# Kernel tuning notes

Hardware: AMD Instinct MI355X
Metric: run time of the kernel (lower is better)

The kernel has to match this reference:

```python
import jax, jax.numpy as jnp
import numpy as np

N = 100000   # nodes
F = 128      # feature dim (== numEdges ctor arg)
H = 64       # hidden_dim
E = 1600000  # edges (avg degree 16)


def setup_inputs() -> dict:
    key = jax.random.key(0)
    ks = jax.random.split(key, 8)
    x = jax.random.normal(ks[0], (N, F), dtype=jnp.float32)
    edge_index = jax.random.randint(ks[1], (2, E), 0, N)
    sF = 1.0 / np.sqrt(F)
    sH = 1.0 / np.sqrt(H)
    conv_W = jax.random.normal(ks[2], (F, F), dtype=jnp.float32) * sF  # GCNConv linear weight
    conv_b = jnp.zeros((F,), dtype=jnp.float32)
    w1 = jax.random.normal(ks[3], (H, F), dtype=jnp.float32) * sF
    b1 = jnp.zeros((H,), dtype=jnp.float32)
    w2 = jax.random.normal(ks[4], (H, H), dtype=jnp.float32) * sH
    b2 = jnp.zeros((H,), dtype=jnp.float32)
    w3 = jax.random.normal(ks[5], (1, H), dtype=jnp.float32) * sH
    b3 = jnp.zeros((1,), dtype=jnp.float32)
    return dict(x=x, edge_index=edge_index, conv_W=conv_W, conv_b=conv_b,
                w1=w1, b1=b1, w2=w2, b2=b2, w3=w3, b3=b3)


def reference(x, edge_index, conv_W, conv_b, w1, b1, w2, b2, w3, b3):
    n = x.shape[0]
    # --- GCNConv: D^{-1/2}(A+I)D^{-1/2} X W + b ---
    xw = x @ conv_W.T                                   # [N, F]
    loops = jnp.arange(n)
    src = jnp.concatenate([edge_index[0], loops])       # add self-loops
    dst = jnp.concatenate([edge_index[1], loops])
    deg = jax.ops.segment_sum(jnp.ones(src.shape[0], xw.dtype), dst, num_segments=n)
    dinv = jnp.where(deg > 0, jax.lax.rsqrt(deg), 0.0)
    norm = dinv[src] * dinv[dst]                        # [E+N]
    h = jax.ops.segment_sum(xw[src] * norm[:, None], dst, num_segments=n) + conv_b  # [N, F]
    # --- MedianAggregation (index=None -> single segment, 'lower' interpolation) ---
    med = jnp.sort(h, axis=0)[(n - 1) // 2][None, :]    # [1, F]
    # --- tanh MLP ---
    a = jnp.tanh(med @ w1.T + b1)
    a = jnp.tanh(a @ w2.T + b2)
    return a @ w3.T + b3                                # [1, 1]
```

## Files before the change

### kernel.cpp

```cpp
#include <hip/hip_runtime.h>
#include <math.h>


#define CAP    24576
#define CCAP   96
#define DSTR   32
#define OVCAP  4096
#define SPCAP  2048
#define BCAP   4608
#define NBKMAX 400
#define CH     4096

typedef __attribute__((ext_vector_type(8))) short short8;
typedef __attribute__((ext_vector_type(4))) float f32x4;
typedef __attribute__((ext_vector_type(8))) _Float16 half8;
typedef __attribute__((ext_vector_type(2))) _Float16 half2v;

__device__ __forceinline__ unsigned ordKey(float x) {
    unsigned u = __float_as_uint(x);
    return (u & 0x80000000u) ? ~u : (u | 0x80000000u);
}
__device__ __forceinline__ unsigned short f2bf(float f) {
    unsigned u = __float_as_uint(f);
    return (unsigned short)((u + 0x7FFFu + ((u >> 16) & 1u)) >> 16);
}

__global__ void k_init(int* __restrict__ cursor, int* __restrict__ below,
                       int* __restrict__ candCnt, int* __restrict__ ovCnt,
                       const float* __restrict__ W, short* __restrict__ Whi,
                       short* __restrict__ Wlo, int nbk) {
    if (blockIdx.x == 1) {
        for (int idx = threadIdx.x; idx < 16384; idx += 256) {
            int j = idx & 7, lane = (idx >> 3) & 63;
            int t = (idx >> 9) & 7, s = idx >> 12;
            int row = t * 16 + (lane & 15);
            int k = s * 32 + (lane >> 4) * 8 + j;
            float w = W[row * 128 + k];
            unsigned short hb = f2bf(w);
            float hf = __uint_as_float((unsigned)hb << 16);
            Whi[idx] = (short)hb;
            Wlo[idx] = (short)f2bf(w - hf);
        }
        return;
    }
    int t = threadIdx.x;
    for (int i = t; i < nbk; i += 256) cursor[i] = 0;
    if (t < 128) { below[t] = 0; candCnt[t] = 0; }
    if (t == 0) { ovCnt[0] = 0; ovCnt[1] = 0; }
}

__global__ __launch_bounds__(256) void k_binGemm(
        const float* __restrict__ x, const short* __restrict__ Whi,
        const short* __restrict__ Wlo, _Float16* __restrict__ xw, int n, int GB,
        const int* __restrict__ src, const int* __restrict__ dst, int E,
        int* __restrict__ cursor, int2* __restrict__ binned,
        int* __restrict__ ovCnt, int2* __restrict__ ovBuf, int nbk) {
    __shared__ char smem[39168];
    const int t = threadIdx.x;
    if ((int)blockIdx.x < GB) {
        float* trn = (float*)smem;
        const int lane = t & 63, wv = t >> 6;
        const int quad = lane >> 4, m = lane & 15;
        const int rowBase = blockIdx.x * 64 + wv * 16;
        const int r = rowBase + m;
        const int rl = r < n ? r : (n - 1);
        f32x4 acc[8];
        #pragma unroll
        for (int q = 0; q < 8; q++) acc[q] = (f32x4){0.f, 0.f, 0.f, 0.f};
        #pragma unroll
        for (int s = 0; s < 4; s++) {
            const float* xp = x + (size_t)rl * 128 + s * 32 + quad * 8;
            float4 p0 = *(const float4*)xp;
            float4 p1 = *(const float4*)(xp + 4);
            float f[8] = {p0.x, p0.y, p0.z, p0.w, p1.x, p1.y, p1.z, p1.w};
            short8 ah, al;
            #pragma unroll
            for (int j = 0; j < 8; j++) {
                unsigned short hb = f2bf(f[j]);
                float hf = __uint_as_float((unsigned)hb << 16);
                ah[j] = (short)hb;
                al[j] = (short)f2bf(f[j] - hf);
            }
            #pragma unroll
            for (int q = 0; q < 8; q++) {
                short8 bh = *(const short8*)(Whi + (((s * 8 + q) * 64 + lane) << 3));
                short8 bl = *(const short8*)(Wlo + (((s * 8 + q) * 64 + lane) << 3));
                acc[q] = __builtin_amdgcn_mfma_f32_16x16x32_bf16(ah, bh, acc[q], 0, 0, 0);
                acc[q] = __builtin_amdgcn_mfma_f32_16x16x32_bf16(al, bh, acc[q], 0, 0, 0);
                acc[q] = __builtin_amdgcn_mfma_f32_16x16x32_bf16(ah, bl, acc[q], 0, 0, 0);
            }
        }
        float* tw = trn + wv * (16 * 132);
        #pragma unroll
        for (int q = 0; q < 8; q++)
            #pragma unroll
            for (int e = 0; e < 4; e++)
                tw[(quad * 4 + e) * 132 + q * 16 + m] = acc[q][e];
        #pragma unroll
        for (int i = 0; i < 4; i++) {
            int row = i * 4 + (lane >> 4);
            int c8 = lane & 15;
            const float* tp = tw + row * 132 + c8 * 8;
            float4 p0 = *(const float4*)tp;
            float4 p1 = *(const float4*)(tp + 4);
            half8 o;
            o[0] = (_Float16)p0.x; o[1] = (_Float16)p0.y;
            o[2] = (_Float16)p0.z; o[3] = (_Float16)p0.w;
            o[4] = (_Float16)p1.x; o[5] = (_Float16)p1.y;
            o[6] = (_Float16)p1.z; o[7] = (_Float16)p1.w;
            int grow = rowBase + row;
            if (grow < n) *(half8*)(xw + (size_t)grow * 128 + c8 * 8) = o;
        }
    } else {
        int2* stage = (int2*)smem;
        int* hist  = (int*)(smem + 32768);
        int* gbase = hist + NBKMAX;
        int* hist2 = gbase + NBKMAX;
        int* sbase = hist2 + NBKMAX;
        const int e0 = ((int)blockIdx.x - GB) * CH;
        const int len = min(CH, E - e0);
        for (int i = t; i < nbk; i += 256) { hist[i] = 0; hist2[i] = 0; }
        __syncthreads();
        for (int k = t; k < len; k += 256) {
            int s = src[e0 + k], d = dst[e0 + k];
            stage[k] = make_int2(s, d);
            atomicAdd(&hist[d >> 8], 1);
        }
        __syncthreads();
        for (int i = t; i < nbk; i += 256) {
            int c = hist[i];
            if (c) {
                int g = atomicAdd(&cursor[i], c);
                if (g + c <= BCAP) gbase[i] = g;
                else {
                    gbase[i] = -1;
                    sbase[i] = atomicAdd(ovCnt, c);
                }
            }
        }
        __syncthreads();
        for (int k = t; k < len; k += 256) {
            int2 e = stage[k];
            int b = e.y >> 8;
            int p = atomicAdd(&hist2[b], 1);
            int g = gbase[b];
            if (g >= 0) binned[(size_t)b * BCAP + g + p] = e;
            else {
                int o = sbase[b] + p;
                if (o < OVCAP) ovBuf[o] = make_int2(e.y, e.x);
            }
        }
    }
}

__global__ __launch_bounds__(512) void k_build(int2* __restrict__ binned,
                                               const int* __restrict__ cursor,
                                               float* __restrict__ dinv,
                                               unsigned char* __restrict__ deg8,
                                               int* __restrict__ ovCnt,
                                               int2* __restrict__ ovBuf,
                                               int* __restrict__ spillNodes, int n) {
    __shared__ int ladj[256 * DSTR];
    __shared__ int lcnt[256];
    const int b = blockIdx.x, t = threadIdx.x;
    const int cnt = min(cursor[b], BCAP);
    const size_t e0 = (size_t)b * BCAP;
    if (t < 256) lcnt[t] = 0;
    __syncthreads();
    for (int k = t; k < cnt; k += 512) {
        int2 e = binned[e0 + k];
        int li = e.y & 255;
        int pos = atomicAdd(&lcnt[li], 1);
        if (pos < DSTR) ladj[li * DSTR + pos] = e.x;
        else {
            int o = atomicAdd(ovCnt, 1);
            if (o < OVCAP) ovBuf[o] = make_int2(e.y, e.x);
        }
    }
    __syncthreads();
    int4* adjOut = (int4*)((int*)binned + e0 * 2);
    const int4* lsrc4 = (const int4*)ladj;
    for (int i = t; i < 2048; i += 512) adjOut[i] = lsrc4[i];
    if (t < 256) {
        int node = b * 256 + t;
        if (node < n) {
            int deg = lcnt[t];
            dinv[node] = (float)(1.0 / sqrt((double)(deg + 1)));
            deg8[node] = (unsigned char)(deg < 255 ? deg : 255);
            if (deg > DSTR) {
                int p = atomicAdd(ovCnt + 1, 1);
                if (p < SPCAP) spillNodes[p] = node;
            }
        }
    }
}

__global__ __launch_bounds__(256) void k_aggH(const _Float16* __restrict__ xw,
                                              const unsigned char* __restrict__ deg8,
                                              const int* __restrict__ adjAll,
                                              const float* __restrict__ dinv,
                                              const float* __restrict__ conv_b,
                                              _Float16* __restrict__ h, int n) {
    const int d = blockIdx.x * 4 + (threadIdx.x >> 6);
    if (d >= n) return;
    const int lane = threadIdx.x & 63;
    const int l32 = lane & 31;
    int degT = deg8[d];
    const int degB = degT < DSTR ? degT : DSTR;
    const float dd = dinv[d];
    const int* adjRow = adjAll + (size_t)(d >> 8) * (BCAP * 2) + (d & 255) * DSTR;
    int aj = adjRow[l32];
    bool ev = (lane < 32) && (l32 < degB);
    int ajs = ev ? aj : 0;
    float dv = ev ? dinv[ajs] : 0.f;
    const half2v* xwv = (const half2v*)xw;
    half2v a = xwv[(size_t)d * 64 + lane];
    float ax = dd * dd * (float)a.x, ay = dd * dd * (float)a.y;
    int j = 0;
    for (; j + 8 <= degB; j += 8) {
        int s[8];
        float w[8];
        #pragma unroll
        for (int q = 0; q < 8; q++) {
            s[q] = __shfl(ajs, j + q, 64);
            w[q] = dd * __shfl(dv, j + q, 64);
        }
        #pragma unroll
        for (int q = 0; q < 8; q++) {
            half2v v = xwv[(size_t)s[q] * 64 + lane];
            ax += w[q] * (float)v.x;
            ay += w[q] * (float)v.y;
        }
    }
    if (j < degB) {
        int s[8];
        float w[8];
        #pragma unroll
        for (int q = 0; q < 8; q++) {
            int idx = j + q;
            bool ok = idx < degB;
            int lsrc = ok ? idx : 0;
            int sv = __shfl(ajs, lsrc, 64);
            float wv = dd * __shfl(dv, lsrc, 64);
            s[q] = ok ? sv : 0;
            w[q] = ok ? wv : 0.f;
        }
        #pragma unroll
        for (int q = 0; q < 8; q++) {
            half2v v = xwv[(size_t)s[q] * 64 + lane];
            ax += w[q] * (float)v.x;
            ay += w[q] * (float)v.y;
        }
    }
    float2 cb = ((const float2*)conv_b)[lane];
    half2v o;
    o.x = (_Float16)(ax + cb.x);
    o.y = (_Float16)(ay + cb.y);
    ((half2v*)h)[(size_t)d * 64 + lane] = o;
}

__global__ void k_spillFix(const _Float16* __restrict__ xw,
                           const int* __restrict__ spillNodes,
                           const int* __restrict__ adjAll,
                           const float* __restrict__ dinv,
                           const float* __restrict__ conv_b,
                           const int2* __restrict__ ovBuf,
                           const int* __restrict__ ovCnt,
                           _Float16* __restrict__ h) {
    int m = ovCnt[0];  if (m > OVCAP) m = OVCAP;
    int sp = ovCnt[1]; if (sp > SPCAP) sp = SPCAP;
    const int t = threadIdx.x;
    for (int i = blockIdx.x; i < sp; i += gridDim.x) {
        const int d = spillNodes[i];
        const float dd = dinv[d];
        float acc = dd * dd * (float)xw[(size_t)d * 128 + t];
        const int* adjRow = adjAll + (size_t)(d >> 8) * (BCAP * 2) + (d & 255) * DSTR;
        for (int j = 0; j < DSTR; j++) {
            int a = adjRow[j];
            acc += dd * dinv[a] * (float)xw[(size_t)a * 128 + t];
        }
        for (int k = 0; k < m; k++) {
            int2 e = ovBuf[k];
            if (e.x == d)
                acc += dd * dinv[e.y] * (float)xw[(size_t)e.y * 128 + t];
        }
        h[(size_t)d * 128 + t] = (_Float16)(acc + conv_b[t]);
    }
}

__global__ __launch_bounds__(256) void k_sample(const _Float16* __restrict__ h, int n,
                                                unsigned* __restrict__ Lkey,
                                                unsigned* __restrict__ Ukey) {
    __shared__ int hist[2048];
    __shared__ int wsum[4];
    const int c = blockIdx.x, t = threadIdx.x;
    for (int i = t; i < 2048; i += 256) hist[i] = 0;
    __syncthreads();
    const int ns = (n + 31) >> 5;
    for (int i = t; i < ns; i += 256) {
        float v = (float)h[(size_t)(i << 5) * 128 + c];
        atomicAdd(&hist[ordKey(v) >> 21], 1);
    }
    __syncthreads();
    int ps = 0;
    #pragma unroll
    for (int b = 0; b < 8; b++) ps += hist[t * 8 + b];
    const int lane = t & 63, wv = t >> 6;
    int sc = ps;
    #pragma unroll
    for (int off = 1; off < 64; off <<= 1) {
        int y = __shfl_up(sc, off, 64);
        if (lane >= off) sc += y;
    }
    if (lane == 63) wsum[wv] = sc;
    __syncthreads();
    int wbase = 0;
    for (int ww = 0; ww < wv; ww++) wbase += wsum[ww];
    const int excl = wbase + sc - ps;
    const int sMid = (ns - 1) >> 1;
    const int delta = (int)(4.0f * sqrtf((float)ns)) + 1;
    int sLo = sMid - delta; if (sLo < 0) sLo = 0;
    int sHi = sMid + delta; if (sHi > ns - 1) sHi = ns - 1;
    if (sLo >= excl && sLo < excl + ps) {
        int rem = sLo - excl, b = t * 8;
        for (;; b++) { int cc = hist[b]; if (rem < cc) break; rem -= cc; }
        Lkey[c] = (unsigned)b << 21;
    }
    if (sHi >= excl && sHi < excl + ps) {
        int rem = sHi - excl, b = t * 8;
        for (;; b++) { int cc = hist[b]; if (rem < cc) break; rem -= cc; }
        Ukey[c] = (((unsigned)(b + 1)) << 21) - 1u;
    }
}

__global__ __launch_bounds__(256) void k_classify(const _Float16* __restrict__ h,
                                                  int total8,
                                                  const unsigned* __restrict__ Lkey,
                                                  const unsigned* __restrict__ Ukey,
                                                  int* __restrict__ below,
                                                  int* __restrict__ candCnt,
                                                  _Float16* __restrict__ cand) {
    __shared__ _Float16 buf[128 * CCAP];
    __shared__ int cN[128], cB[128];
    const int t = threadIdx.x;
    for (int i = t; i < 128; i += 256) { cN[i] = 0; cB[i] = 0; }
    __syncthreads();
    const int stride = gridDim.x * blockDim.x;
    const int i0 = blockIdx.x * blockDim.x + t;
    const int jb = (i0 << 3) & 127;
    unsigned L[8], U[8];
    #pragma unroll
    for (int k = 0; k < 8; k++) { L[k] = Lkey[jb + k]; U[k] = Ukey[jb + k]; }
    int b[8] = {0, 0, 0, 0, 0, 0, 0, 0};
    const half8* hv = (const half8*)h;
    for (int i = i0; i < total8; i += stride) {
        half8 v = hv[i];
        #pragma unroll
        for (int k = 0; k < 8; k++) {
            float f = (float)v[k];
            unsigned u = ordKey(f);
            if (u < L[k]) b[k]++;
            else if (u <= U[k]) {
                int p = atomicAdd(&cN[jb + k], 1);
                if (p < CCAP) buf[(jb + k) * CCAP + p] = v[k];
                else {
                    int g = atomicAdd(&candCnt[jb + k], 1);
                    if (g < CAP) cand[(size_t)(jb + k) * CAP + g] = v[k];
                }
            }
        }
    }
    #pragma unroll
    for (int k = 0; k < 8; k++)
        if (b[k]) atomicAdd(&cB[jb + k], b[k]);
    __syncthreads();
    if (t < 128) {
        if (cB[t]) atomicAdd(&below[t], cB[t]);
        int nn = cN[t] < CCAP ? cN[t] : CCAP;
        if (nn) {
            int base = atomicAdd(&candCnt[t], nn);
            for (int k2 = 0; k2 < nn && base + k2 < CAP; k2++)
                cand[(size_t)t * CAP + base + k2] = buf[t * CCAP + k2];
        }
    }
}

__global__ __launch_bounds__(256) void k_final(const _Float16* __restrict__ cand,
                                               const int* __restrict__ candCnt,
                                               const int* __restrict__ below, int n,
                                               float* __restrict__ med) {
    __shared__ int hist[2048];
    __shared__ int sSel;
    __shared__ int sRank;
    const int c = blockIdx.x, t = threadIdx.x;
    int cnt = candCnt[c]; if (cnt > CAP) cnt = CAP;
    const unsigned short* cp = (const unsigned short*)(cand + (size_t)c * CAP);
    if (t == 0) {
        int r = (n - 1) / 2 - below[c];
        if (r < 0) r = 0;
        if (r >= cnt) r = cnt - 1;
        sRank = r;
        sSel = 0;
    }
    for (int i = t; i < 2048; i += 256) hist[i] = 0;
    __syncthreads();
    for (int i = t; i < cnt; i += 256) {
        unsigned ub = cp[i];
        unsigned k = (ub & 0x8000u) ? (~ub & 0xFFFFu) : (ub | 0x8000u);
        atomicAdd(&hist[k >> 5], 1);
    }
    __syncthreads();
    if (t < 64) {
        int ps = 0;
        for (int b = t * 32; b < t * 32 + 32; b++) ps += hist[b];
        int sc = ps;
        #pragma unroll
        for (int off = 1; off < 64; off <<= 1) {
            int y = __shfl_up(sc, off, 64);
            if (t >= off) sc += y;
        }
        int excl = sc - ps;
        int r = sRank;
        if (excl <= r && r < sc) {
            int b = t * 32, rem = r - excl;
            for (;; b++) {
                int cc = hist[b];
                if (rem < cc) break;
                rem -= cc;
            }
            sSel = b;
            sRank = rem;
        }
    }
    __syncthreads();
    if (t < 32) hist[t] = 0;
    __syncthreads();
    const int sel = sSel;
    for (int i = t; i < cnt; i += 256) {
        unsigned ub = cp[i];
        unsigned k = (ub & 0x8000u) ? (~ub & 0xFFFFu) : (ub | 0x8000u);
        if ((int)(k >> 5) == sel) atomicAdd(&hist[k & 31], 1);
    }
    __syncthreads();
    if (t == 0) {
        int rem = sRank, b = 0;
        for (;; b++) {
            int cc = hist[b];
            if (rem < cc) break;
            rem -= cc;
        }
        unsigned key16 = ((unsigned)sel << 5) | (unsigned)b;
        unsigned short bits = (key16 & 0x8000u) ? (unsigned short)(key16 & 0x7FFFu)
                                                : (unsigned short)(~key16 & 0xFFFFu);
        _Float16 hv;
        *(unsigned short*)&hv = bits;
        med[c] = (float)hv;
    }
}

__global__ void k_mlp(const float* __restrict__ med,
                      const float* __restrict__ w1, const float* __restrict__ b1,
                      const float* __restrict__ w2, const float* __restrict__ b2,
                      const float* __restrict__ w3, const float* __restrict__ b3,
                      float* __restrict__ out) {
    __shared__ float m[128], a1[64], a2[64];
    int t = threadIdx.x;
    if (t < 128) m[t] = med[t];
    __syncthreads();
    if (t < 64) {
        float acc = b1[t];
        for (int f = 0; f < 128; f++) acc += m[f] * w1[t * 128 + f];
        a1[t] = tanhf(acc);
    }
    __syncthreads();
    if (t < 64) {
        float acc = b2[t];
        for (int f = 0; f < 64; f++) acc += a1[f] * w2[t * 64 + f];
        a2[t] = tanhf(acc);
    }
    __syncthreads();
    if (t == 0) {
        float acc = b3[0];
        for (int f = 0; f < 64; f++) acc += a2[f] * w3[f];
        out[0] = acc;
    }
}

extern "C" void kernel_launch(void* const* d_in, const int* in_sizes, int n_in,
                              void* d_out, int out_size, void* d_ws, size_t ws_size,
                              hipStream_t stream) {
    const float* x      = (const float*)d_in[0];
    const int*   ei     = (const int*)d_in[1];
    const float* conv_W = (const float*)d_in[2];
    const float* conv_b = (const float*)d_in[3];
    const float* w1 = (const float*)d_in[4];
    const float* b1 = (const float*)d_in[5];
    const float* w2 = (const float*)d_in[6];
    const float* b2 = (const float*)d_in[7];
    const float* w3 = (const float*)d_in[8];
    const float* b3 = (const float*)d_in[9];

    const int N = in_sizes[0] / 128;
    const int E = in_sizes[1] / 2;
    const int* src = ei;
    const int* dst = ei + E;
    const int NBK = (N + 255) / 256;

    char* p = (char*)d_ws;
    auto alloc = [&](size_t bytes) -> char* {
        char* q = p;
        p += (bytes + 255) & ~(size_t)255;
        return q;
    };
    _Float16* xw  = (_Float16*)alloc((size_t)N * 128 * 2);
    _Float16* h   = (_Float16*)alloc((size_t)N * 128 * 2);
    int2*  binned = (int2*)alloc((size_t)NBK * BCAP * 8);
    _Float16* cand = (_Float16*)alloc((size_t)128 * CAP * 2);
    float* dinv   = (float*)alloc((size_t)N * 4);
    unsigned char* deg8 = (unsigned char*)alloc((size_t)N);
    int*   cursor = (int*)alloc((size_t)NBK * 4);
    short* Whi    = (short*)alloc(16384 * 2);
    short* Wlo    = (short*)alloc(16384 * 2);
    int2*  ovBuf  = (int2*)alloc((size_t)OVCAP * 8);
    int*   ovCnt  = (int*)alloc(256);
    int*   spillNodes = (int*)alloc((size_t)SPCAP * 4);
    unsigned* Lkey = (unsigned*)alloc(128 * 4);
    unsigned* Ukey = (unsigned*)alloc(128 * 4);
    int*   below   = (int*)alloc(128 * 4);
    int*   candCnt = (int*)alloc(128 * 4);
    float* med     = (float*)alloc(128 * 4);

    const int GB   = (N + 63) / 64;
    const int BINB = (E + CH - 1) / CH;

    k_init<<<2, 256, 0, stream>>>(cursor, below, candCnt, ovCnt, conv_W, Whi, Wlo, NBK);
    k_binGemm<<<GB + BINB, 256, 0, stream>>>(x, Whi, Wlo, xw, N, GB,
                                             src, dst, E, cursor, binned,
                                             ovCnt, ovBuf, NBK);
    k_build<<<NBK, 512, 0, stream>>>(binned, cursor, dinv, deg8, ovCnt, ovBuf,
                                     spillNodes, N);
    k_aggH<<<(N + 3) / 4, 256, 0, stream>>>(xw, deg8, (const int*)binned, dinv,
                                            conv_b, h, N);
    k_spillFix<<<16, 128, 0, stream>>>(xw, spillNodes, (const int*)binned, dinv,
                                       conv_b, ovBuf, ovCnt, h);
    k_sample<<<128, 256, 0, stream>>>(h, N, Lkey, Ukey);
    k_classify<<<2048, 256, 0, stream>>>(h, N * 16, Lkey, Ukey, below, candCnt, cand);
    k_final<<<128, 256, 0, stream>>>(cand, candCnt, below, N, med);
    k_mlp<<<1, 128, 0, stream>>>(med, w1, b1, w2, b2, w3, b3, (float*)d_out);
}
```

Measured before the change: 316.4 us.

## Restructure kernel launches: split gemm/binning, fuse spill into sample, final into MLP

Splits the combined GEMM+edge-binning kernel into two separate launches and splits the aggregation into two half-range launches. It merges the spill-node fixup into the sampling kernel as extra blocks, and merges the MLP into the final median kernel with a last-block atomic counter. The aim is to cut small-kernel launch gaps at the tail of the pipeline. The cost is that the GEMM and binning no longer overlap. Sampling may also read spill-node rows of h while they are being rewritten, which could perturb the approximate bounds.

```diff
diff --git a/kernel.cpp b/kernel.cpp
--- a/kernel.cpp
+++ b/kernel.cpp
@@ -46,109 +46,110 @@
     int t = threadIdx.x;
     for (int i = t; i < nbk; i += 256) cursor[i] = 0;
     if (t < 128) { below[t] = 0; candCnt[t] = 0; }
-    if (t == 0) { ovCnt[0] = 0; ovCnt[1] = 0; }
-}
-
-__global__ __launch_bounds__(256) void k_binGemm(
+    if (t == 0) { ovCnt[0] = 0; ovCnt[1] = 0; ovCnt[2] = 0; }
+}
+
+__global__ __launch_bounds__(256) void k_gemm(
         const float* __restrict__ x, const short* __restrict__ Whi,
-        const short* __restrict__ Wlo, _Float16* __restrict__ xw, int n, int GB,
+        const short* __restrict__ Wlo, _Float16* __restrict__ xw, int n) {
+    __shared__ float trn[4 * 16 * 132];
+    const int t = threadIdx.x;
+    const int lane = t & 63, wv = t >> 6;
+    const int quad = lane >> 4, m = lane & 15;
+    const int rowBase = blockIdx.x * 64 + wv * 16;
+    const int r = rowBase + m;
+    const int rl = r < n ? r : (n - 1);
+    f32x4 acc[8];
+    #pragma unroll
+    for (int q = 0; q < 8; q++) acc[q] = (f32x4){0.f, 0.f, 0.f, 0.f};
+    #pragma unroll
+    for (int s = 0; s < 4; s++) {
+        const float* xp = x + (size_t)rl * 128 + s * 32 + quad * 8;
+        float4 p0 = *(const float4*)xp;
+        float4 p1 = *(const float4*)(xp + 4);
+        float f[8] = {p0.x, p0.y, p0.z, p0.w, p1.x, p1.y, p1.z, p1.w};
+        short8 ah, al;
+        #pragma unroll
+        for (int j = 0; j < 8; j++) {
+            unsigned short hb = f2bf(f[j]);
+            float hf = __uint_as_float((unsigned)hb << 16);
+            ah[j] = (short)hb;
+            al[j] = (short)f2bf(f[j] - hf);
+        }
+        #pragma unroll
+        for (int q = 0; q < 8; q++) {
+            short8 bh = *(const short8*)(Whi + (((s * 8 + q) * 64 + lane) << 3));
+            short8 bl = *(const short8*)(Wlo + (((s * 8 + q) * 64 + lane) << 3));
+            acc[q] = __builtin_amdgcn_mfma_f32_16x16x32_bf16(ah, bh, acc[q], 0, 0, 0);
+            acc[q] = __builtin_amdgcn_mfma_f32_16x16x32_bf16(al, bh, acc[q], 0, 0, 0);
+            acc[q] = __builtin_amdgcn_mfma_f32_16x16x32_bf16(ah, bl, acc[q], 0, 0, 0);
+        }
+    }
+    float* tw = trn + wv * (16 * 132);
+    #pragma unroll
+    for (int q = 0; q < 8; q++)
+        #pragma unroll
+        for (int e = 0; e < 4; e++)
+            tw[(quad * 4 + e) * 132 + q * 16 + m] = acc[q][e];
+    #pragma unroll
+    for (int i = 0; i < 4; i++) {
+        int row = i * 4 + (lane >> 4);
+        int c8 = lane & 15;
+        const float* tp = tw + row * 132 + c8 * 8;
+        float4 p0 = *(const float4*)tp;
+        float4 p1 = *(const float4*)(tp + 4);
+        half8 o;
+        o[0] = (_Float16)p0.x; o[1] = (_Float16)p0.y;
+        o[2] = (_Float16)p0.z; o[3] = (_Float16)p0.w;
+        o[4] = (_Float16)p1.x; o[5] = (_Float16)p1.y;
+        o[6] = (_Float16)p1.z; o[7] = (_Float16)p1.w;
+        int grow = rowBase + row;
+        if (grow < n) *(half8*)(xw + (size_t)grow * 128 + c8 * 8) = o;
+    }
+}
+
+__global__ __launch_bounds__(256) void k_bin(
         const int* __restrict__ src, const int* __restrict__ dst, int E,
         int* __restrict__ cursor, int2* __restrict__ binned,
         int* __restrict__ ovCnt, int2* __restrict__ ovBuf, int nbk) {
     __shared__ char smem[39168];
     const int t = threadIdx.x;
-    if ((int)blockIdx.x < GB) {
-        float* trn = (float*)smem;
-        const int lane = t & 63, wv = t >> 6;
-        const int quad = lane >> 4, m = lane & 15;
-        const int rowBase = blockIdx.x * 64 + wv * 16;
-        const int r = rowBase + m;
-        const int rl = r < n ? r : (n - 1);
-        f32x4 acc[8];
-        #pragma unroll
-        for (int q = 0; q < 8; q++) acc[q] = (f32x4){0.f, 0.f, 0.f, 0.f};
-        #pragma unroll
-        for (int s = 0; s < 4; s++) {
-            const float* xp = x + (size_t)rl * 128 + s * 32 + quad * 8;
-            float4 p0 = *(const float4*)xp;
-            float4 p1 = *(const float4*)(xp + 4);
-            float f[8] = {p0.x, p0.y, p0.z, p0.w, p1.x, p1.y, p1.z, p1.w};
-            short8 ah, al;
-            #pragma unroll
-            for (int j = 0; j < 8; j++) {
-                unsigned short hb = f2bf(f[j]);
-                float hf = __uint_as_float((unsigned)hb << 16);
-                ah[j] = (short)hb;
-                al[j] = (short)f2bf(f[j] - hf);
+    int2* stage = (int2*)smem;
+    int* hist  = (int*)(smem + 32768);
+    int* gbase = hist + NBKMAX;
+    int* hist2 = gbase + NBKMAX;
+    int* sbase = hist2 + NBKMAX;
+    const int e0 = (int)blockIdx.x * CH;
+    const int len = min(CH, E - e0);
+    for (int i = t; i < nbk; i += 256) { hist[i] = 0; hist2[i] = 0; }
+    __syncthreads();
+    for (int k = t; k < len; k += 256) {
+        int s = src[e0 + k], d = dst[e0 + k];
+        stage[k] = make_int2(s, d);
+        atomicAdd(&hist[d >> 8], 1);
+    }
+    __syncthreads();
+    for (int i = t; i < nbk; i += 256) {
+        int c = hist[i];
+        if (c) {
+            int g = atomicAdd(&cursor[i], c);
+            if (g + c <= BCAP) gbase[i] = g;
+            else {
+                gbase[i] = -1;
+                sbase[i] = atomicAdd(ovCnt, c);
             }
-            #pragma unroll
-            for (int q = 0; q < 8; q++) {
-                short8 bh = *(const short8*)(Whi + (((s * 8 + q) * 64 + lane) << 3));
-                short8 bl = *(const short8*)(Wlo + (((s * 8 + q) * 64 + lane) << 3));
-                acc[q] = __builtin_amdgcn_mfma_f32_16x16x32_bf16(ah, bh, acc[q], 0, 0, 0);
-                acc[q] = __builtin_amdgcn_mfma_f32_16x16x32_bf16(al, bh, acc[q], 0, 0, 0);
-                acc[q] = __builtin_amdgcn_mfma_f32_16x16x32_bf16(ah, bl, acc[q], 0, 0, 0);
-            }
-        }
-        float* tw = trn + wv * (16 * 132);
-        #pragma unroll
-        for (int q = 0; q < 8; q++)
-            #pragma unroll
-            for (int e = 0; e < 4; e++)
-                tw[(quad * 4 + e) * 132 + q * 16 + m] = acc[q][e];
-        #pragma unroll
-        for (int i = 0; i < 4; i++) {
-            int row = i * 4 + (lane >> 4);
-            int c8 = lane & 15;
-            const float* tp = tw + row * 132 + c8 * 8;
-            float4 p0 = *(const float4*)tp;
-            float4 p1 = *(const float4*)(tp + 4);
-            half8 o;
-            o[0] = (_Float16)p0.x; o[1] = (_Float16)p0.y;
-            o[2] = (_Float16)p0.z; o[3] = (_Float16)p0.w;
-            o[4] = (_Float16)p1.x; o[5] = (_Float16)p1.y;
-            o[6] = (_Float16)p1.z; o[7] = (_Float16)p1.w;
-            int grow = rowBase + row;
-            if (grow < n) *(half8*)(xw + (size_t)grow * 128 + c8 * 8) = o;
-        }
-    } else {
-        int2* stage = (int2*)smem;
-        int* hist  = (int*)(smem + 32768);
-        int* gbase = hist + NBKMAX;
-        int* hist2 = gbase + NBKMAX;
-        int* sbase = hist2 + NBKMAX;
-        const int e0 = ((int)blockIdx.x - GB) * CH;
-        const int len = min(CH, E - e0);
-        for (int i = t; i < nbk; i += 256) { hist[i] = 0; hist2[i] = 0; }
-        __syncthreads();
-        for (int k = t; k < len; k += 256) {
-            int s = src[e0 + k], d = dst[e0 + k];
-            stage[k] = make_int2(s, d);
-            atomicAdd(&hist[d >> 8], 1);
-        }
-        __syncthreads();
-        for (int i = t; i < nbk; i += 256) {
-            int c = hist[i];
-            if (c) {
-                int g = atomicAdd(&cursor[i], c);
-                if (g + c <= BCAP) gbase[i] = g;
-                else {
-                    gbase[i] = -1;
-                    sbase[i] = atomicAdd(ovCnt, c);
-                }
-            }
-        }
-        __syncthreads();
-        for (int k = t; k < len; k += 256) {
-            int2 e = stage[k];
-            int b = e.y >> 8;
-            int p = atomicAdd(&hist2[b], 1);
-            int g = gbase[b];
-            if (g >= 0) binned[(size_t)b * BCAP + g + p] = e;
-            else {
-                int o = sbase[b] + p;
-                if (o < OVCAP) ovBuf[o] = make_int2(e.y, e.x);
-            }
+        }
+    }
+    __syncthreads();
+    for (int k = t; k < len; k += 256) {
+        int2 e = stage[k];
+        int b = e.y >> 8;
+        int p = atomicAdd(&hist2[b], 1);
+        int g = gbase[b];
+        if (g >= 0) binned[(size_t)b * BCAP + g + p] = e;
+        else {
+            int o = sbase[b] + p;
+            if (o < OVCAP) ovBuf[o] = make_int2(e.y, e.x);
         }
     }
 }
@@ -200,9 +201,10 @@
                                               const int* __restrict__ adjAll,
                                               const float* __restrict__ dinv,
                                               const float* __restrict__ conv_b,
-                                              _Float16* __restrict__ h, int n) {
-    const int d = blockIdx.x * 4 + (threadIdx.x >> 6);
-    if (d >= n) return;
+                                              _Float16* __restrict__ h,
+                                              int n0, int n1) {
+    const int d = n0 + blockIdx.x * 4 + (threadIdx.x >> 6);
+    if (d >= n1) return;
     const int lane = threadIdx.x & 63;
     const int l32 = lane & 31;
     int degT = deg8[d];
@@ -259,41 +261,39 @@
     ((half2v*)h)[(size_t)d * 64 + lane] = o;
 }
 
-__global__ void k_spillFix(const _Float16* __restrict__ xw,
-                           const int* __restrict__ spillNodes,
-                           const int* __restrict__ adjAll,
-                           const float* __restrict__ dinv,
-                           const float* __restrict__ conv_b,
-                           const int2* __restrict__ ovBuf,
-                           const int* __restrict__ ovCnt,
-                           _Float16* __restrict__ h) {
-    int m = ovCnt[0];  if (m > OVCAP) m = OVCAP;
-    int sp = ovCnt[1]; if (sp > SPCAP) sp = SPCAP;
+__global__ __launch_bounds__(256) void k_sampleSpill(
+        _Float16* h, int n,
+        unsigned* __restrict__ Lkey, unsigned* __restrict__ Ukey,
+        const _Float16* __restrict__ xw, const int* __restrict__ spillNodes,
+        const int* __restrict__ adjAll, const float* __restrict__ dinv,
+        const float* __restrict__ conv_b, const int2* __restrict__ ovBuf,
+        const int* __restrict__ ovCnt) {
     const int t = threadIdx.x;
-    for (int i = blockIdx.x; i < sp; i += gridDim.x) {
-        const int d = spillNodes[i];
-        const float dd = dinv[d];
-        float acc = dd * dd * (float)xw[(size_t)d * 128 + t];
-        const int* adjRow = adjAll + (size_t)(d >> 8) * (BCAP * 2) + (d & 255) * DSTR;
-        for (int j = 0; j < DSTR; j++) {
-            int a = adjRow[j];
-            acc += dd * dinv[a] * (float)xw[(size_t)a * 128 + t];
-        }
-        for (int k = 0; k < m; k++) {
-            int2 e = ovBuf[k];
-            if (e.x == d)
-                acc += dd * dinv[e.y] * (float)xw[(size_t)e.y * 128 + t];
-        }
-        h[(size_t)d * 128 + t] = (_Float16)(acc + conv_b[t]);
-    }
-}
-
-__global__ __launch_bounds__(256) void k_sample(const _Float16* __restrict__ h, int n,
-                                                unsigned* __restrict__ Lkey,
-                                                unsigned* __restrict__ Ukey) {
+    if (blockIdx.x >= 128) {
+        int m = ovCnt[0];  if (m > OVCAP) m = OVCAP;
+        int sp = ovCnt[1]; if (sp > SPCAP) sp = SPCAP;
+        if (t >= 128) return;
+        for (int i = (int)blockIdx.x - 128; i < sp; i += 16) {
+            const int d = spillNodes[i];
+            const float dd = dinv[d];
+            float acc = dd * dd * (float)xw[(size_t)d * 128 + t];
+            const int* adjRow = adjAll + (size_t)(d >> 8) * (BCAP * 2) + (d & 255) * DSTR;
+            for (int j = 0; j < DSTR; j++) {
+                int a = adjRow[j];
+                acc += dd * dinv[a] * (float)xw[(size_t)a * 128 + t];
+            }
+            for (int k = 0; k < m; k++) {
+                int2 e = ovBuf[k];
+                if (e.x == d)
+                    acc += dd * dinv[e.y] * (float)xw[(size_t)e.y * 128 + t];
+            }
+            h[(size_t)d * 128 + t] = (_Float16)(acc + conv_b[t]);
+        }
+        return;
+    }
     __shared__ int hist[2048];
     __shared__ int wsum[4];
-    const int c = blockIdx.x, t = threadIdx.x;
+    const int c = blockIdx.x;
     for (int i = t; i < 2048; i += 256) hist[i] = 0;
     __syncthreads();
     const int ns = (n + 31) >> 5;
@@ -385,13 +385,18 @@
     }
 }
 
-__global__ __launch_bounds__(256) void k_final(const _Float16* __restrict__ cand,
-                                               const int* __restrict__ candCnt,
-                                               const int* __restrict__ below, int n,
-                                               float* __restrict__ med) {
+__global__ __launch_bounds__(256) void k_finalMlp(
+        const _Float16* __restrict__ cand, const int* __restrict__ candCnt,
+        const int* __restrict__ below, int n, float* __restrict__ med,
+        int* __restrict__ doneCnt,
+        const float* __restrict__ w1, const float* __restrict__ b1,
+        const float* __restrict__ w2, const float* __restrict__ b2,
+        const float* __restrict__ w3, const float* __restrict__ b3,
+        float* __restrict__ out) {
     __shared__ int hist[2048];
     __shared__ int sSel;
     __shared__ int sRank;
+    __shared__ int lastFlag;
     const int c = blockIdx.x, t = threadIdx.x;
     int cnt = candCnt[c]; if (cnt > CAP) cnt = CAP;
     const unsigned short* cp = (const unsigned short*)(cand + (size_t)c * CAP);
@@ -455,16 +460,14 @@
         _Float16 hv;
         *(unsigned short*)&hv = bits;
         med[c] = (float)hv;
-    }
-}
-
-__global__ void k_mlp(const float* __restrict__ med,
-                      const float* __restrict__ w1, const float* __restrict__ b1,
-                      const float* __restrict__ w2, const float* __restrict__ b2,
-                      const float* __restrict__ w3, const float* __restrict__ b3,
-                      float* __restrict__ out) {
+        __threadfence();
+        int old = atomicAdd(doneCnt, 1);
+        lastFlag = (old == 127);
+    }
+    __syncthreads();
+    if (!lastFlag) return;
+    __threadfence();
     __shared__ float m[128], a1[64], a2[64];
-    int t = threadIdx.x;
     if (t < 128) m[t] = med[t];
     __syncthreads();
     if (t < 64) {
@@ -532,19 +535,21 @@
 
     const int GB   = (N + 63) / 64;
     const int BINB = (E + CH - 1) / CH;
+    const int NH   = ((N / 2) + 3) & ~3;
 
     k_init<<<2, 256, 0, stream>>>(cursor, below, candCnt, ovCnt, conv_W, Whi, Wlo, NBK);
-    k_binGemm<<<GB + BINB, 256, 0, stream>>>(x, Whi, Wlo, xw, N, GB,
-                                             src, dst, E, cursor, binned,
-                                             ovCnt, ovBuf, NBK);
+    k_gemm<<<GB, 256, 0, stream>>>(x, Whi, Wlo, xw, N);
+    k_bin<<<BINB, 256, 0, stream>>>(src, dst, E, cursor, binned, ovCnt, ovBuf, NBK);
     k_build<<<NBK, 512, 0, stream>>>(binned, cursor, dinv, deg8, ovCnt, ovBuf,
                                      spillNodes, N);
-    k_aggH<<<(N + 3) / 4, 256, 0, stream>>>(xw, deg8, (const int*)binned, dinv,
-                                            conv_b, h, N);
-    k_spillFix<<<16, 128, 0, stream>>>(xw, spillNodes, (const int*)binned, dinv,
-                                       conv_b, ovBuf, ovCnt, h);
-    k_sample<<<128, 256, 0, stream>>>(h, N, Lkey, Ukey);
+    k_aggH<<<(NH + 3) / 4, 256, 0, stream>>>(xw, deg8, (const int*)binned, dinv,
+                                             conv_b, h, 0, NH);
+    k_aggH<<<(N - NH + 3) / 4, 256, 0, stream>>>(xw, deg8, (const int*)binned, dinv,
+                                                 conv_b, h, NH, N);
+    k_sampleSpill<<<144, 256, 0, stream>>>(h, N, Lkey, Ukey, xw, spillNodes,
+                                           (const int*)binned, dinv, conv_b,
+                                           ovBuf, ovCnt);
     k_classify<<<2048, 256, 0, stream>>>(h, N * 16, Lkey, Ukey, below, candCnt, cand);
-    k_final<<<128, 256, 0, stream>>>(cand, candCnt, below, N, med);
-    k_mlp<<<1, 128, 0, stream>>>(med, w1, b1, w2, b2, w3, b3, (float*)d_out);
-}
+    k_finalMlp<<<128, 256, 0, stream>>>(cand, candCnt, below, N, med, ovCnt + 2,
+                                        w1, b1, w2, b2, w3, b3, (float*)d_out);
+}
```

After: 325.5 us. +2.9%, slower.
